# Performance work log

Hardware: AMD Instinct MI355X
Metric: run time of the kernel (lower is better)

The kernel has to match this reference:

```python
import jax, jax.numpy as jnp
import numpy as np

N_NODES = 100000
N_EDGES = 1600000
D_IN, D_H, D_OUT = 512, 128, 64
BN_EPS = 1e-5


def setup_inputs() -> dict:
    key = jax.random.key(0)
    ks = jax.random.split(key, 8)
    x = jax.random.normal(ks[0], (N_NODES, D_IN), dtype=jnp.float32)
    # COO sparse normalized adjacency
    row = jnp.sort(jax.random.randint(ks[1], (N_EDGES,), 0, N_NODES))
    col = jax.random.randint(ks[2], (N_EDGES,), 0, N_NODES)
    adj_vals = jax.random.uniform(ks[3], (N_EDGES,), dtype=jnp.float32) / 16.0
    # GraphConvolution params (xavier_uniform weight, zero bias)
    lim0 = float(np.sqrt(6.0 / (D_IN + D_H)))
    lim1 = float(np.sqrt(6.0 / (D_H + D_OUT)))
    W0 = jax.random.uniform(ks[4], (D_IN, D_H), minval=-lim0, maxval=lim0, dtype=jnp.float32)
    W1 = jax.random.uniform(ks[5], (D_H, D_OUT), minval=-lim1, maxval=lim1, dtype=jnp.float32)
    b0 = jnp.zeros((D_H,), dtype=jnp.float32)
    b1 = jnp.zeros((D_OUT,), dtype=jnp.float32)
    return {"x": x, "W0": W0, "b0": b0, "W1": W1, "b1": b1,
            "adj_vals": adj_vals, "row": row, "col": col}


def _spmm(vals, row, col, h, n):
    # (sparse adj) @ h : gather source rows, scale by edge value, scatter-add to dest
    return jax.ops.segment_sum(vals[:, None] * h[col], row, num_segments=n)


def reference(x, W0, b0, W1, b1, adj_vals, row, col):
    n = x.shape[0]
    # layer 0: adj @ (x @ W0) + b0  (dropout is identity in eval mode)
    h = _spmm(adj_vals, row, col, x @ W0, n) + b0
    h = jax.nn.relu(h)
    # BatchNorm1d(affine=False, track_running_stats=False): batch stats, biased var
    mean = jnp.mean(h, axis=0)
    var = jnp.mean(jnp.square(h - mean), axis=0)
    h = (h - mean) * jax.lax.rsqrt(var + BN_EPS)
    # layer 1: adj @ (h @ W1) + b1
    return _spmm(adj_vals, row, col, h @ W1, n) + b1
```

## Files before the change

### kernel.cpp

```cpp
#include <hip/hip_runtime.h>
#include <hip/hip_bf16.h>
#include <cstdint>
#include <cstddef>

#define D_IN  512
#define D_H   128
#define D_OUT 64
#define SB    256

typedef __attribute__((ext_vector_type(8))) short bf16x8;
typedef __attribute__((ext_vector_type(4))) float f32x4;

__device__ __forceinline__ float bf2f(unsigned short u) {
  union { unsigned int i; float f; } v; v.i = ((unsigned int)u) << 16; return v.f;
}
__device__ __forceinline__ unsigned short f2bf(float f) {
  union { unsigned int i; float f; } v; v.f = f;
  unsigned int r = v.i + 0x7FFFu + ((v.i >> 16) & 1u);
  return (unsigned short)(r >> 16);
}
__device__ __forceinline__ unsigned int pk_bf16(float a, float b) {
  union { __hip_bfloat162 h; unsigned int u; } cv;
  cv.h = __float22bfloat162_rn(make_float2(a, b));
  return cv.u;
}

#define OFF_RP    0u
#define OFF_W0T   400384u
#define OFF_W1TP  531456u
#define OFF_CVEC  547840u
#define OFF_PSUM  548096u
#define OFF_PSQ   679168u
#define OFF_H     810240u
#define END_H     26410240u
#define END_HW    39210240u

__global__ void k_init(const int* __restrict__ row, int* __restrict__ rp,
                       const float* __restrict__ W0, unsigned short* __restrict__ W0t,
                       int n, int e, int RB) {
  int b = blockIdx.x, t = threadIdx.x;
  if (b < RB) {
    int i = b * 256 + t;
    if (i > n) return;
    int lo = 0, hi = e;
    while (lo < hi) { int mid = (lo + hi) >> 1; if (row[mid] < i) lo = mid + 1; else hi = mid; }
    rp[i] = lo;
  } else {
    int idx = (b - RB) * 256 + t;
    int k = idx & (D_IN - 1);
    int nn = idx >> 9;
    W0t[nn * D_IN + k] = f2bf(W0[k * D_H + nn]);
  }
}

__global__ __launch_bounds__(256) void k_gemm1(const float* __restrict__ A,
                                               const unsigned short* __restrict__ Bt,
                                               unsigned short* __restrict__ C, int M) {
  __shared__ unsigned short Ash[2][4096];
  __shared__ unsigned short Bsh[2][4096];
  const int tid = threadIdx.x, lane = tid & 63, wave = tid >> 6;
  const int wm = (wave >> 1) * 64, wn = (wave & 1) * 64;
  const int m0 = blockIdx.x * 128, quad = lane >> 4, l16 = lane & 15;
  f32x4 acc[4][4] = {};
  int am[2], ak[2];
  const float* aptr[2];
  const unsigned short* bptr[2];
#pragma unroll
  for (int i = 0; i < 2; ++i) {
    int c = tid + i * 256;
    am[i] = c >> 2; ak[i] = c & 3;
    int gm = m0 + am[i]; if (gm >= M) gm = M - 1;
    aptr[i] = A + (size_t)gm * D_IN + ak[i] * 8;
    bptr[i] = Bt + (size_t)am[i] * D_IN + ak[i] * 8;
  }
  f32x4 areg[2][2]; bf16x8 breg[2];
#pragma unroll
  for (int i = 0; i < 2; ++i) {
    areg[i][0] = *(const f32x4*)(aptr[i]);
    areg[i][1] = *(const f32x4*)(aptr[i] + 4);
    breg[i]    = *(const bf16x8*)(bptr[i]);
  }
  const int NIT = D_IN / 32;
  for (int it = 0; it < NIT; ++it) {
    const int buf = it & 1;
    unsigned short* ash = Ash[buf];
    unsigned short* bsh = Bsh[buf];
#pragma unroll
    for (int i = 0; i < 2; ++i) {
      unsigned int pk4[4];
      pk4[0] = pk_bf16(areg[i][0][0], areg[i][0][1]);
      pk4[1] = pk_bf16(areg[i][0][2], areg[i][0][3]);
      pk4[2] = pk_bf16(areg[i][1][0], areg[i][1][1]);
      pk4[3] = pk_bf16(areg[i][1][2], areg[i][1][3]);
      *(uint4*)&ash[(ak[i] * 128 + am[i]) * 8] = *(uint4*)pk4;
      *(bf16x8*)&bsh[(ak[i] * 128 + am[i]) * 8] = breg[i];
    }
    __syncthreads();
    if (it + 1 < NIT) {
      int k0 = (it + 1) * 32;
#pragma unroll
      for (int i = 0; i < 2; ++i) {
        areg[i][0] = *(const f32x4*)(aptr[i] + k0);
        areg[i][1] = *(const f32x4*)(aptr[i] + k0 + 4);
        breg[i]    = *(const bf16x8*)(bptr[i] + k0);
      }
    }
    bf16x8 af[4], bfv[4];
#pragma unroll
    for (int mf = 0; mf < 4; ++mf)
      af[mf] = *(const bf16x8*)&ash[(quad * 128 + (wm + mf * 16 + l16)) * 8];
#pragma unroll
    for (int nf = 0; nf < 4; ++nf)
      bfv[nf] = *(const bf16x8*)&bsh[(quad * 128 + (wn + nf * 16 + l16)) * 8];
#pragma unroll
    for (int mf = 0; mf < 4; ++mf)
#pragma unroll
      for (int nf = 0; nf < 4; ++nf)
        acc[mf][nf] = __builtin_amdgcn_mfma_f32_16x16x32_bf16(af[mf], bfv[nf], acc[mf][nf], 0, 0, 0);
  }
#pragma unroll
  for (int mf = 0; mf < 4; ++mf)
#pragma unroll
    for (int nf = 0; nf < 4; ++nf)
#pragma unroll
      for (int i = 0; i < 4; ++i) {
        int r = m0 + wm + mf * 16 + quad * 4 + i;
        int cc = wn + nf * 16 + l16;
        if (r < M) C[(size_t)r * D_H + cc] = f2bf(acc[mf][nf][i]);
      }
}

__global__ __launch_bounds__(256) void k_spmm1(const unsigned int* __restrict__ xw2,
                                               const float* __restrict__ adj,
                                               const int* __restrict__ col,
                                               const int* __restrict__ rp,
                                               const float* __restrict__ b0,
                                               unsigned int* __restrict__ h2, int n) {
  int node = blockIdx.x * 4 + (threadIdx.x >> 6);
  if (node >= n) return;
  int l = threadIdx.x & 63;
  int e0 = rp[node], e1 = rp[node + 1];
  float a0 = 0.f, a1 = 0.f;
  for (int e = e0; e < e1; e += 8) {
    int ee = e + (l & 7);
    int ec = ee < e1 ? ee : e1 - 1;
    int   cl = col[ec];
    float vl = ee < e1 ? adj[ec] : 0.f;
#pragma unroll
    for (int j = 0; j < 8; ++j) {
      int   cj = __shfl(cl, j, 64);
      float wj = __shfl(vl, j, 64);
      unsigned int p = xw2[(size_t)cj * 64 + l];
      a0 += wj * bf2f((unsigned short)(p & 0xFFFF));
      a1 += wj * bf2f((unsigned short)(p >> 16));
    }
  }
  float r0 = fmaxf(a0 + b0[2 * l], 0.f);
  float r1 = fmaxf(a1 + b0[2 * l + 1], 0.f);
  h2[(size_t)node * 64 + l] = ((unsigned int)f2bf(r1) << 16) | (unsigned int)f2bf(r0);
}

__global__ __launch_bounds__(256) void k_stats(const unsigned int* __restrict__ h2,
                                               float* __restrict__ psum,
                                               float* __restrict__ psq, int n) {
  __shared__ float sA[256], sB[256], qA[256], qB[256];
  int t = threadIdx.x;
  int f2 = t & 63, rg = t >> 6;
  float s0 = 0.f, s1 = 0.f, q0 = 0.f, q1 = 0.f;
  for (int r = blockIdx.x * 4 + rg; r < n; r += gridDim.x * 4) {
    unsigned int p = h2[(size_t)r * 64 + f2];
    float v0 = bf2f((unsigned short)(p & 0xFFFF));
    float v1 = bf2f((unsigned short)(p >> 16));
    s0 += v0; s1 += v1; q0 += v0 * v0; q1 += v1 * v1;
  }
  sA[t] = s0; sB[t] = s1; qA[t] = q0; qB[t] = q1;
  __syncthreads();
  if (t < 64) {
    float S0 = sA[t] + sA[t + 64] + sA[t + 128] + sA[t + 192];
    float S1 = sB[t] + sB[t + 64] + sB[t + 128] + sB[t + 192];
    float Q0 = qA[t] + qA[t + 64] + qA[t + 128] + qA[t + 192];
    float Q1 = qB[t] + qB[t + 64] + qB[t + 128] + qB[t + 192];
    psum[blockIdx.x * 128 + 2 * t]     = S0;
    psum[blockIdx.x * 128 + 2 * t + 1] = S1;
    psq [blockIdx.x * 128 + 2 * t]     = Q0;
    psq [blockIdx.x * 128 + 2 * t + 1] = Q1;
  }
}

__global__ void k_prep2(const float* __restrict__ psum, const float* __restrict__ psq,
                        const float* __restrict__ W1,
                        unsigned short* __restrict__ W1tp, float* __restrict__ cvec, int n) {
  __shared__ float rs[256], rq[256];
  __shared__ float mean_s[128], istd_s[128];
  __shared__ float cpart[256];
  int t = threadIdx.x;
  int f = t & 127, half = t >> 7;
  {
    float s = 0.f, q = 0.f;
#pragma unroll 8
    for (int b = half * (SB / 2); b < (half + 1) * (SB / 2); ++b) {
      s += psum[b * 128 + f]; q += psq[b * 128 + f];
    }
    rs[t] = s; rq[t] = q;
  }
  __syncthreads();
  if (t < 128) {
    float s = rs[t] + rs[t + 128];
    float q = rq[t] + rq[t + 128];
    float m = s / (float)n;
    float var = q / (float)n - m * m;
    if (var < 0.f) var = 0.f;
    mean_s[t] = m;
    istd_s[t] = rsqrtf(var + 1e-5f);
  }
  __syncthreads();
  for (int idx = t; idx < D_OUT * D_H; idx += 256) {
    int nn = idx >> 7, k = idx & 127;
    W1tp[nn * D_H + k] = f2bf(istd_s[k] * W1[k * D_OUT + nn]);
  }
  {
    int o = t & 63, part = t >> 6;
    float a = 0.f;
    for (int k = part * 32; k < part * 32 + 32; ++k)
      a += mean_s[k] * istd_s[k] * W1[k * D_OUT + o];
    cpart[t] = a;
  }
  __syncthreads();
  if (t < D_OUT)
    cvec[t] = -(cpart[t] + cpart[t + 64] + cpart[t + 128] + cpart[t + 192]);
}

__global__ __launch_bounds__(256) void k_gemm2(const unsigned short* __restrict__ A,
                                               const unsigned short* __restrict__ Bt,
                                               const float* __restrict__ cvec,
                                               unsigned short* __restrict__ Cout, int M) {
  __shared__ unsigned short Ash[4096];
  __shared__ unsigned short Bsh[2048];
  const int tid = threadIdx.x, lane = tid & 63, wave = tid >> 6;
  const int wm = wave * 32, m0 = blockIdx.x * 128;
  const int quad = lane >> 4, l16 = lane & 15;
  f32x4 acc[2][4] = {};
  for (int k0 = 0; k0 < D_H; k0 += 32) {
    __syncthreads();
#pragma unroll
    for (int i = 0; i < 2; ++i) {
      int c = tid + i * 256;
      int m = c >> 2, k8 = c & 3;
      int gm = m0 + m; if (gm >= M) gm = M - 1;
      *(bf16x8*)&Ash[(k8 * 128 + m) * 8] = *(const bf16x8*)&A[(size_t)gm * D_H + k0 + k8 * 8];
    }
    {
      int nn = tid >> 2, k8 = tid & 3;
      *(bf16x8*)&Bsh[(k8 * 64 + nn) * 8] = *(const bf16x8*)&Bt[(size_t)nn * D_H + k0 + k8 * 8];
    }
    __syncthreads();
    bf16x8 af[2], bfv[4];
#pragma unroll
    for (int mf = 0; mf < 2; ++mf)
      af[mf] = *(const bf16x8*)&Ash[(quad * 128 + (wm + mf * 16 + l16)) * 8];
#pragma unroll
    for (int nf = 0; nf < 4; ++nf)
      bfv[nf] = *(const bf16x8*)&Bsh[(quad * 64 + (nf * 16 + l16)) * 8];
#pragma unroll
    for (int mf = 0; mf < 2; ++mf)
#pragma unroll
      for (int nf = 0; nf < 4; ++nf)
        acc[mf][nf] = __builtin_amdgcn_mfma_f32_16x16x32_bf16(af[mf], bfv[nf], acc[mf][nf], 0, 0, 0);
  }
#pragma unroll
  for (int mf = 0; mf < 2; ++mf)
#pragma unroll
    for (int nf = 0; nf < 4; ++nf)
#pragma unroll
      for (int i = 0; i < 4; ++i) {
        int r = m0 + wm + mf * 16 + quad * 4 + i;
        int cc = nf * 16 + l16;
        if (r < M) Cout[(size_t)r * 64 + cc] = f2bf(acc[mf][nf][i] + cvec[cc]);
      }
}

__global__ __launch_bounds__(256) void k_spmm2(const unsigned int* __restrict__ hw2,
                                               const float* __restrict__ adj,
                                               const int* __restrict__ col,
                                               const int* __restrict__ rp,
                                               const float* __restrict__ b1,
                                               float2* __restrict__ o2, int n) {
  int node = blockIdx.x * 8 + (threadIdx.x >> 5);
  if (node >= n) return;
  int l = threadIdx.x & 31;
  int e0 = rp[node], e1 = rp[node + 1];
  float a0 = 0.f, a1 = 0.f;
  for (int e = e0; e < e1; e += 8) {
    int ee = e + (l & 7);
    int ec = ee < e1 ? ee : e1 - 1;
    int   cl = col[ec];
    float vl = ee < e1 ? adj[ec] : 0.f;
#pragma unroll
    for (int j = 0; j < 8; ++j) {
      int   cj = __shfl(cl, j, 32);
      float wj = __shfl(vl, j, 32);
      unsigned int p = hw2[(size_t)cj * 32 + l];
      a0 += wj * bf2f((unsigned short)(p & 0xFFFF));
      a1 += wj * bf2f((unsigned short)(p >> 16));
    }
  }
  float2 r; r.x = a0 + b1[2 * l]; r.y = a1 + b1[2 * l + 1];
  o2[(size_t)node * 32 + l] = r;
}

extern "C" void kernel_launch(void* const* d_in, const int* in_sizes, int n_in,
                              void* d_out, int out_size, void* d_ws, size_t ws_size,
                              hipStream_t stream) {
  const float* x   = (const float*)d_in[0];
  const float* W0  = (const float*)d_in[1];
  const float* b0  = (const float*)d_in[2];
  const float* W1  = (const float*)d_in[3];
  const float* b1  = (const float*)d_in[4];
  const float* adj = (const float*)d_in[5];
  const int* row = (const int*)d_in[6];
  const int* col = (const int*)d_in[7];
  const int N = in_sizes[0] / D_IN;
  const int E = in_sizes[5];

  char* ws = (char*)d_ws;
  int*            rp   = (int*)(ws + OFF_RP);
  unsigned short* W0t  = (unsigned short*)(ws + OFF_W0T);
  unsigned short* W1tp = (unsigned short*)(ws + OFF_W1TP);
  float*          cvec = (float*)(ws + OFF_CVEC);
  float*          psum = (float*)(ws + OFF_PSUM);
  float*          psq  = (float*)(ws + OFF_PSQ);
  unsigned short* h    = (unsigned short*)(ws + OFF_H);

  unsigned short* xw = (unsigned short*)d_out;
  const bool hw_in_ws = (ws_size >= (size_t)END_HW);
  unsigned short* hwp  = hw_in_ws ? (unsigned short*)(ws + END_H) : (unsigned short*)d_out;
  float*          outd = hw_in_ws ? (float*)d_out                 : (float*)(ws + OFF_H);

  const int RB = (N + 1 + 255) / 256;
  const int TB = (D_IN * D_H) / 256;
  k_init<<<RB + TB, 256, 0, stream>>>(row, rp, W0, W0t, N, E, RB);
  k_gemm1<<<(N + 127) / 128, 256, 0, stream>>>(x, W0t, xw, N);
  k_spmm1<<<(N + 3) / 4, 256, 0, stream>>>((const unsigned int*)xw, adj, col, rp, b0,
                                           (unsigned int*)h, N);
  k_stats<<<SB, 256, 0, stream>>>((const unsigned int*)h, psum, psq, N);
  k_prep2<<<1, 256, 0, stream>>>(psum, psq, W1, W1tp, cvec, N);
  k_gemm2<<<(N + 127) / 128, 256, 0, stream>>>(h, W1tp, cvec, hwp, N);
  k_spmm2<<<(N + 7) / 8, 256, 0, stream>>>((const unsigned int*)hwp, adj, col, rp, b1,
                                           (float2*)outd, N);
  if (!hw_in_ws) {
    hipMemcpyAsync(d_out, outd, (size_t)N * D_OUT * sizeof(float),
                   hipMemcpyDeviceToDevice, stream);
  }
}
```

Measured before the change: 478.0 us.

## Split SpMM edges across lane groups with 16-byte gathers and shuffle reduction

Both SpMM kernels are restructured so each wavefront splits a node's edges across lane groups (4 groups of 16 lanes for layer 1, 8 groups of 8 lanes for layer 2). Each lane gathers 8 bf16 features with one 16-byte load instead of 4-byte loads, and the groups are combined with xor-shuffle reductions. This is meant to issue more independent, wider gathers per lane and drop the per-edge broadcast shuffles, raising memory-level parallelism on the latency-bound irregular gathers. The cost is more accumulator registers, a cross-lane reduction per node, and idle lanes during the final write. The second SpMM also moves from 32 to 64 lanes per node.

Measured after the change: 491.9 us. 1.03x slower.

```diff
diff --git a/kernel.cpp b/kernel.cpp
--- a/kernel.cpp
+++ b/kernel.cpp
@@ -130,6 +130,17 @@
       }
 }
 
+#define ACCP(P, W) { \
+  union { unsigned int u; float f; } _t; \
+  _t.u = (P).x << 16;         a0 += (W) * _t.f; \
+  _t.u = (P).x & 0xFFFF0000u; a1 += (W) * _t.f; \
+  _t.u = (P).y << 16;         a2 += (W) * _t.f; \
+  _t.u = (P).y & 0xFFFF0000u; a3 += (W) * _t.f; \
+  _t.u = (P).z << 16;         a4 += (W) * _t.f; \
+  _t.u = (P).z & 0xFFFF0000u; a5 += (W) * _t.f; \
+  _t.u = (P).w << 16;         a6 += (W) * _t.f; \
+  _t.u = (P).w & 0xFFFF0000u; a7 += (W) * _t.f; }
+
 __global__ __launch_bounds__(256) void k_spmm1(const unsigned int* __restrict__ xw2,
                                                const float* __restrict__ adj,
                                                const int* __restrict__ col,
@@ -138,26 +149,47 @@
                                                unsigned int* __restrict__ h2, int n) {
   int node = blockIdx.x * 4 + (threadIdx.x >> 6);
   if (node >= n) return;
-  int l = threadIdx.x & 63;
-  int e0 = rp[node], e1 = rp[node + 1];
-  float a0 = 0.f, a1 = 0.f;
-  for (int e = e0; e < e1; e += 8) {
-    int ee = e + (l & 7);
-    int ec = ee < e1 ? ee : e1 - 1;
-    int   cl = col[ec];
-    float vl = ee < e1 ? adj[ec] : 0.f;
-#pragma unroll
-    for (int j = 0; j < 8; ++j) {
-      int   cj = __shfl(cl, j, 64);
-      float wj = __shfl(vl, j, 64);
-      unsigned int p = xw2[(size_t)cj * 64 + l];
-      a0 += wj * bf2f((unsigned short)(p & 0xFFFF));
-      a1 += wj * bf2f((unsigned short)(p >> 16));
-    }
-  }
-  float r0 = fmaxf(a0 + b0[2 * l], 0.f);
-  float r1 = fmaxf(a1 + b0[2 * l + 1], 0.f);
-  h2[(size_t)node * 64 + l] = ((unsigned int)f2bf(r1) << 16) | (unsigned int)f2bf(r0);
+  const int l = threadIdx.x & 63;
+  const int q = l >> 4, s = l & 15;
+  const int e0 = rp[node], e1 = rp[node + 1];
+  float a0 = 0.f, a1 = 0.f, a2 = 0.f, a3 = 0.f;
+  float a4 = 0.f, a5 = 0.f, a6 = 0.f, a7 = 0.f;
+  int e = e0;
+  for (; e + 16 <= e1; e += 16) {
+    int eb = e + 4 * q;
+    int   c0 = col[eb],     c1 = col[eb + 1], c2 = col[eb + 2], c3 = col[eb + 3];
+    float w0 = adj[eb],     w1 = adj[eb + 1], w2 = adj[eb + 2], w3 = adj[eb + 3];
+    uint4 p0 = *(const uint4*)(xw2 + (size_t)c0 * 64 + 4 * s);
+    uint4 p1 = *(const uint4*)(xw2 + (size_t)c1 * 64 + 4 * s);
+    uint4 p2 = *(const uint4*)(xw2 + (size_t)c2 * 64 + 4 * s);
+    uint4 p3 = *(const uint4*)(xw2 + (size_t)c3 * 64 + 4 * s);
+    ACCP(p0, w0); ACCP(p1, w1); ACCP(p2, w2); ACCP(p3, w3);
+  }
+  for (; e < e1; e += 4) {
+    int idx = e + q;
+    int ic = idx < e1 ? idx : e1 - 1;
+    int   c = col[ic];
+    float w = idx < e1 ? adj[ic] : 0.f;
+    uint4 p = *(const uint4*)(xw2 + (size_t)c * 64 + 4 * s);
+    ACCP(p, w);
+  }
+#define RED2(v) { v += __shfl_xor(v, 16, 64); v += __shfl_xor(v, 32, 64); }
+  RED2(a0) RED2(a1) RED2(a2) RED2(a3) RED2(a4) RED2(a5) RED2(a6) RED2(a7)
+#undef RED2
+  if (q == 0) {
+    float4 bl = *(const float4*)(b0 + 8 * s);
+    float4 bh = *(const float4*)(b0 + 8 * s + 4);
+    float r0 = fmaxf(a0 + bl.x, 0.f), r1 = fmaxf(a1 + bl.y, 0.f);
+    float r2 = fmaxf(a2 + bl.z, 0.f), r3 = fmaxf(a3 + bl.w, 0.f);
+    float r4 = fmaxf(a4 + bh.x, 0.f), r5 = fmaxf(a5 + bh.y, 0.f);
+    float r6 = fmaxf(a6 + bh.z, 0.f), r7 = fmaxf(a7 + bh.w, 0.f);
+    uint4 o;
+    o.x = ((unsigned int)f2bf(r1) << 16) | (unsigned int)f2bf(r0);
+    o.y = ((unsigned int)f2bf(r3) << 16) | (unsigned int)f2bf(r2);
+    o.z = ((unsigned int)f2bf(r5) << 16) | (unsigned int)f2bf(r4);
+    o.w = ((unsigned int)f2bf(r7) << 16) | (unsigned int)f2bf(r6);
+    *(uint4*)(h2 + (size_t)node * 64 + 4 * s) = o;
+  }
 }
 
 __global__ __launch_bounds__(256) void k_stats(const unsigned int* __restrict__ h2,
@@ -284,28 +316,43 @@
                                                const int* __restrict__ col,
                                                const int* __restrict__ rp,
                                                const float* __restrict__ b1,
-                                               float2* __restrict__ o2, int n) {
-  int node = blockIdx.x * 8 + (threadIdx.x >> 5);
+                                               float* __restrict__ outp, int n) {
+  int node = blockIdx.x * 4 + (threadIdx.x >> 6);
   if (node >= n) return;
-  int l = threadIdx.x & 31;
-  int e0 = rp[node], e1 = rp[node + 1];
-  float a0 = 0.f, a1 = 0.f;
-  for (int e = e0; e < e1; e += 8) {
-    int ee = e + (l & 7);
-    int ec = ee < e1 ? ee : e1 - 1;
-    int   cl = col[ec];
-    float vl = ee < e1 ? adj[ec] : 0.f;
-#pragma unroll
-    for (int j = 0; j < 8; ++j) {
-      int   cj = __shfl(cl, j, 32);
-      float wj = __shfl(vl, j, 32);
-      unsigned int p = hw2[(size_t)cj * 32 + l];
-      a0 += wj * bf2f((unsigned short)(p & 0xFFFF));
-      a1 += wj * bf2f((unsigned short)(p >> 16));
-    }
-  }
-  float2 r; r.x = a0 + b1[2 * l]; r.y = a1 + b1[2 * l + 1];
-  o2[(size_t)node * 32 + l] = r;
+  const int l = threadIdx.x & 63;
+  const int g = l >> 3, s = l & 7;
+  const int e0 = rp[node], e1 = rp[node + 1];
+  float a0 = 0.f, a1 = 0.f, a2 = 0.f, a3 = 0.f;
+  float a4 = 0.f, a5 = 0.f, a6 = 0.f, a7 = 0.f;
+  int e = e0;
+  for (; e + 16 <= e1; e += 16) {
+    int eb = e + 2 * g;
+    int   c0 = col[eb],  c1 = col[eb + 1];
+    float w0 = adj[eb],  w1 = adj[eb + 1];
+    uint4 p0 = *(const uint4*)(hw2 + (size_t)c0 * 32 + 4 * s);
+    uint4 p1 = *(const uint4*)(hw2 + (size_t)c1 * 32 + 4 * s);
+    ACCP(p0, w0); ACCP(p1, w1);
+  }
+  for (; e < e1; e += 8) {
+    int idx = e + g;
+    int ic = idx < e1 ? idx : e1 - 1;
+    int   c = col[ic];
+    float w = idx < e1 ? adj[ic] : 0.f;
+    uint4 p = *(const uint4*)(hw2 + (size_t)c * 32 + 4 * s);
+    ACCP(p, w);
+  }
+#define RED3(v) { v += __shfl_xor(v, 8, 64); v += __shfl_xor(v, 16, 64); v += __shfl_xor(v, 32, 64); }
+  RED3(a0) RED3(a1) RED3(a2) RED3(a3) RED3(a4) RED3(a5) RED3(a6) RED3(a7)
+#undef RED3
+  if (g == 0) {
+    float4 bl = *(const float4*)(b1 + 8 * s);
+    float4 bh = *(const float4*)(b1 + 8 * s + 4);
+    float4 r0, r1;
+    r0.x = a0 + bl.x; r0.y = a1 + bl.y; r0.z = a2 + bl.z; r0.w = a3 + bl.w;
+    r1.x = a4 + bh.x; r1.y = a5 + bh.y; r1.z = a6 + bh.z; r1.w = a7 + bh.w;
+    *(float4*)(outp + (size_t)node * 64 + 8 * s)     = r0;
+    *(float4*)(outp + (size_t)node * 64 + 8 * s + 4) = r1;
+  }
 }
 
 extern "C" void kernel_launch(void* const* d_in, const int* in_sizes, int n_in,
@@ -345,8 +392,8 @@
   k_stats<<<SB, 256, 0, stream>>>((const unsigned int*)h, psum, psq, N);
   k_prep2<<<1, 256, 0, stream>>>(psum, psq, W1, W1tp, cvec, N);
   k_gemm2<<<(N + 127) / 128, 256, 0, stream>>>(h, W1tp, cvec, hwp, N);
-  k_spmm2<<<(N + 7) / 8, 256, 0, stream>>>((const unsigned int*)hwp, adj, col, rp, b1,
-                                           (float2*)outd, N);
+  k_spmm2<<<(N + 3) / 4, 256, 0, stream>>>((const unsigned int*)hwp, adj, col, rp, b1,
+                                           outd, N);
   if (!hw_in_ws) {
     hipMemcpyAsync(d_out, outd, (size_t)N * D_OUT * sizeof(float),
                    hipMemcpyDeviceToDevice, stream);
```
